# Kernel optimization log

Hardware: AMD Instinct MI355X
Metric: run time of the kernel (lower is better)

The kernel has to match this reference:

```python
import jax, jax.numpy as jnp
import numpy as np

NUM_LATENT = 1024
LATENT_DIM = 256
BETA = 0.25
N_TOKENS = 65536


def setup_inputs() -> dict:
    key = jax.random.key(0)
    k1, k2 = jax.random.split(key)
    latent_embedding = jax.random.normal(k1, (N_TOKENS, LATENT_DIM), dtype=jnp.float32)
    # torch.nn.init.uniform_(codebook, -1/num_latent, 1/num_latent)
    codebook = jax.random.uniform(
        k2, (NUM_LATENT, LATENT_DIM), dtype=jnp.float32,
        minval=-1.0 / NUM_LATENT, maxval=1.0 / NUM_LATENT)
    return {"latent_embedding": latent_embedding, "codebook": codebook}


def reference(latent_embedding, codebook):
    le_det = jax.lax.stop_gradient(latent_embedding)  # [N, D]
    # distances[n,k] = ||z_n||^2 + ||c_k||^2 - 2 z_n . c_k   (z detached, codebook NOT)
    distances = (jnp.sum(le_det ** 2, axis=1, keepdims=True)
                 + jnp.sum(codebook ** 2, axis=1)
                 - 2.0 * jnp.matmul(le_det, codebook.T))  # [N, K]
    encoding_inds = jnp.argmin(distances, axis=1)  # [N]
    # one_hot @ codebook == gather rows of codebook
    quantized_latents = codebook[encoding_inds]  # [N, D]
    num_latent = codebook.shape[0]
    commitment_loss = jnp.mean((jax.lax.stop_gradient(quantized_latents)
                                - latent_embedding) ** 2) * num_latent
    embedding_loss = jnp.mean((quantized_latents - le_det) ** 2) * num_latent
    vq_loss = embedding_loss + commitment_loss * BETA
    probs = jax.nn.softmax(-distances, axis=1)  # [N, K]
    probs = jnp.clip(jnp.mean(probs, axis=0, keepdims=True), 0.001, 0.999)  # [1, K]
    return (quantized_latents, codebook, probs, vq_loss)
```

## Files before the change

kernel.cpp:

```cpp
#include <hip/hip_runtime.h>

#define N_TOK 65536
#define DIM   256
#define K_CODES 1024
#define CB_OFF    16777216
#define PROBS_OFF (16777216 + 262144)
#define LOSS_OFF  (16777216 + 262144 + 1024)
#define TM 64
#define NBLK (N_TOK / TM)

typedef float  f32x4  __attribute__((ext_vector_type(4)));
typedef short  s16x8  __attribute__((ext_vector_type(8)));

__device__ __forceinline__ unsigned short f32_to_bf16(float x) {
    unsigned u = __float_as_uint(x);
    unsigned r = (u + 0x7FFFu + ((u >> 16) & 1u)) >> 16;
    return (unsigned short)r;
}
__device__ __forceinline__ unsigned fkey(float a) {
    unsigned u = __float_as_uint(a);
    unsigned m = (unsigned)(((int)u) >> 31);
    return u ^ (m | 0x80000000u);
}
__device__ __forceinline__ float fkey_inv(unsigned k) {
    unsigned u = (k & 0x80000000u) ? (k ^ 0x80000000u) : ~k;
    return __uint_as_float(u);
}

__device__ __forceinline__ unsigned red16_max_u(unsigned v) {
    unsigned t;
    t = (unsigned)__builtin_amdgcn_update_dpp(0, (int)v, 0xB1,  0xF, 0xF, true); v = v > t ? v : t;
    t = (unsigned)__builtin_amdgcn_update_dpp(0, (int)v, 0x4E,  0xF, 0xF, true); v = v > t ? v : t;
    t = (unsigned)__builtin_amdgcn_update_dpp(0, (int)v, 0x141, 0xF, 0xF, true); v = v > t ? v : t;
    t = (unsigned)__builtin_amdgcn_update_dpp(0, (int)v, 0x140, 0xF, 0xF, true); v = v > t ? v : t;
    return v;
}
__device__ __forceinline__ float red16_sum_f(float v) {
    float t;
    t = __uint_as_float((unsigned)__builtin_amdgcn_update_dpp(0, (int)__float_as_uint(v), 0xB1,  0xF, 0xF, true)); v += t;
    t = __uint_as_float((unsigned)__builtin_amdgcn_update_dpp(0, (int)__float_as_uint(v), 0x4E,  0xF, 0xF, true)); v += t;
    t = __uint_as_float((unsigned)__builtin_amdgcn_update_dpp(0, (int)__float_as_uint(v), 0x141, 0xF, 0xF, true)); v += t;
    t = __uint_as_float((unsigned)__builtin_amdgcn_update_dpp(0, (int)__float_as_uint(v), 0x140, 0xF, 0xF, true)); v += t;
    return v;
}

__global__ __launch_bounds__(512) void k_prep(const float* __restrict__ cb,
                                              float* __restrict__ c2,
                                              unsigned short* __restrict__ cbf,
                                              float* __restrict__ probs_part,
                                              float* __restrict__ lossR,
                                              float* __restrict__ outcb,
                                              int zcount, int nloss, int docopy) {
    const int g  = blockIdx.x;
    const int t  = threadIdx.x;
    const int wv = t >> 6;
    const int ln = t & 63;
    const int l15 = ln & 15, q = ln >> 4;

    const float* zp = cb + (size_t)(g * 16 + l15) * DIM + wv * 32 + q * 8;
    f32x4 z0 = *(const f32x4*)(zp);
    f32x4 z1 = *(const f32x4*)(zp + 4);
    s16x8 a;
    a[0] = (short)f32_to_bf16(z0[0]); a[1] = (short)f32_to_bf16(z0[1]);
    a[2] = (short)f32_to_bf16(z0[2]); a[3] = (short)f32_to_bf16(z0[3]);
    a[4] = (short)f32_to_bf16(z1[0]); a[5] = (short)f32_to_bf16(z1[1]);
    a[6] = (short)f32_to_bf16(z1[2]); a[7] = (short)f32_to_bf16(z1[3]);
    *(s16x8*)(cbf + (size_t)(g * 8 + wv) * 512 + ln * 8) = a;

    float s = z0[0]*z0[0] + z0[1]*z0[1] + z0[2]*z0[2] + z0[3]*z0[3]
            + z1[0]*z1[0] + z1[1]*z1[1] + z1[2]*z1[2] + z1[3]*z1[3];
    s += __shfl_xor(s, 16, 64);
    s += __shfl_xor(s, 32, 64);
    __shared__ float c2p[8][16];
    if (q == 0) c2p[wv][l15] = s;

    const int base = g * 512 + t;
    if (base < nloss) lossR[base] = 0.f;
    if (zcount >= 0) {
        if (base < zcount) probs_part[base] = 0.f;
        if (base + 32768 < zcount) probs_part[base + 32768] = 0.f;
    } else {
        if (base < -zcount) probs_part[(size_t)base * 1024] = 0.f;
    }
    if (docopy) {
        #pragma unroll
        for (int i = 0; i < 8; i++) outcb[base + i * 32768] = cb[base + i * 32768];
    }

    __syncthreads();
    if (t < 16) {
        float acc = 0.f;
        #pragma unroll
        for (int ww = 0; ww < 8; ww++) acc += c2p[ww][t];
        c2[g * 16 + t] = acc;
    }
}

__global__ __launch_bounds__(1024, 4) void k_main(const float* __restrict__ z,
                                                  const float* __restrict__ cb,
                                                  const unsigned short* __restrict__ cbf,
                                                  const float* __restrict__ c2,
                                                  float* __restrict__ out_q,
                                                  float* __restrict__ probs_part,
                                                  float* __restrict__ lossR,
                                                  int repmask) {
    const int t   = threadIdx.x;
    const int w   = t >> 6;
    const int ln  = t & 63;
    const int q   = ln >> 4;
    const int l15 = ln & 15;
    const int k0  = w * 64;
    const int n0  = blockIdx.x * TM;
    float* pp = probs_part +
        (size_t)((repmask < 0) ? (int)blockIdx.x : (int)(blockIdx.x & repmask)) * K_CODES;

    __shared__ unsigned short a_lds[32 * 64 * 8];
    __shared__ float    z2p[32][16];
    __shared__ unsigned kred[16][64];
    __shared__ float    ered[16][64];
    __shared__ int   fidx[64];
    __shared__ float fU[64];

    #pragma unroll
    for (int rep = 0; rep < 2; rep++) {
        const int f   = t + rep * 1024;
        const int md  = w + rep * 16;
        const int m   = md >> 3;
        const int dsv = md & 7;
        const int row = m * 16 + l15;
        const int dim = dsv * 32 + q * 8;
        const float* zp = z + (size_t)(n0 + row) * DIM + dim;
        f32x4 z0 = *(const f32x4*)(zp);
        f32x4 z1 = *(const f32x4*)(zp + 4);
        s16x8 a;
        a[0] = (short)f32_to_bf16(z0[0]); a[1] = (short)f32_to_bf16(z0[1]);
        a[2] = (short)f32_to_bf16(z0[2]); a[3] = (short)f32_to_bf16(z0[3]);
        a[4] = (short)f32_to_bf16(z1[0]); a[5] = (short)f32_to_bf16(z1[1]);
        a[6] = (short)f32_to_bf16(z1[2]); a[7] = (short)f32_to_bf16(z1[3]);
        *(s16x8*)(a_lds + (size_t)f * 8) = a;
        float s = z0[0]*z0[0] + z0[1]*z0[1] + z0[2]*z0[2] + z0[3]*z0[3]
                + z1[0]*z1[0] + z1[1]*z1[1] + z1[2]*z1[2] + z1[3]*z1[3];
        s += __shfl_xor(s, 16, 64);
        s += __shfl_xor(s, 32, 64);
        if (q == 0) z2p[md][l15] = s;
    }

    float c2v[4];
    #pragma unroll
    for (int nt = 0; nt < 4; nt++) c2v[nt] = c2[k0 + nt * 16 + l15];
    f32x4 acc[4][4];
    #pragma unroll
    for (int m = 0; m < 4; m++)
        #pragma unroll
        for (int nt = 0; nt < 4; nt++) {
            const float iv = -0.5f * c2v[nt];
            f32x4 v4 = {iv, iv, iv, iv};
            acc[m][nt] = v4;
        }

    __syncthreads();

    const unsigned short* bb = cbf + (size_t)(w * 4) * 8 * 512 + ln * 8;
    #pragma unroll
    for (int ds = 0; ds < 8; ds++) {
        s16x8 af[4];
        #pragma unroll
        for (int m = 0; m < 4; m++)
            af[m] = *(const s16x8*)(a_lds + (size_t)((m * 8 + ds) * 64 + ln) * 8);
        #pragma unroll
        for (int nt = 0; nt < 4; nt++) {
            s16x8 b = *(const s16x8*)(bb + (size_t)(nt * 8 + ds) * 512);
            #pragma unroll
            for (int m = 0; m < 4; m++)
                acc[m][nt] = __builtin_amdgcn_mfma_f32_16x16x32_bf16(af[m], b, acc[m][nt], 0, 0, 0);
        }
    }

    unsigned lkey[4][4];
    float    lesum[4][4];
    #pragma unroll
    for (int m = 0; m < 4; m++)
        #pragma unroll
        for (int v = 0; v < 4; v++) { lkey[m][v] = 0u; lesum[m][v] = 0.f; }

    #pragma unroll
    for (int m = 0; m < 4; m++)
        #pragma unroll
        for (int nt = 0; nt < 4; nt++) {
            const unsigned colc = 1023u - (unsigned)(k0 + nt * 16 + l15);
            #pragma unroll
            for (int v = 0; v < 4; v++) {
                float a = acc[m][nt][v];
                unsigned key = (fkey(a) & 0xFFFFFC00u) | colc;
                lkey[m][v] = max(lkey[m][v], key);
                float e = __expf(a + a);
                acc[m][nt][v] = e;
                lesum[m][v] += e;
            }
        }

    #pragma unroll
    for (int m = 0; m < 4; m++)
        #pragma unroll
        for (int v = 0; v < 4; v++) {
            lkey[m][v]  = red16_max_u(lkey[m][v]);
            lesum[m][v] = red16_sum_f(lesum[m][v]);
        }

    if (l15 == 0) {
        #pragma unroll
        for (int m = 0; m < 4; m++)
            #pragma unroll
            for (int v = 0; v < 4; v++) {
                const int r = m * 16 + q * 4 + v;
                kred[w][r] = lkey[m][v]; ered[w][r] = lesum[m][v];
            }
    }
    __syncthreads();
    float lossreg = 0.f;
    if (t < 64) {
        unsigned bk = kred[0][t];
        float U = ered[0][t];
        #pragma unroll
        for (int ww = 1; ww < 16; ww++) {
            bk = max(bk, kred[ww][t]);
            U += ered[ww][t];
        }
        fidx[t] = 1023 - (int)(bk & 1023u);
        fU[t] = U;
        float a_rec = fkey_inv(bk);
        float z2 = 0.f;
        #pragma unroll
        for (int ds = 0; ds < 8; ds++) z2 += z2p[(t >> 4) * 8 + ds][t & 15];
        lossreg = z2 - 2.0f * a_rec;
    }
    __syncthreads();

    float ps[4];
    #pragma unroll
    for (int nt = 0; nt < 4; nt++) ps[nt] = 0.f;
    #pragma unroll
    for (int m = 0; m < 4; m++)
        #pragma unroll
        for (int v = 0; v < 4; v++) {
            const float invU = 1.0f / fU[m * 16 + q * 4 + v];
            #pragma unroll
            for (int nt = 0; nt < 4; nt++) ps[nt] += acc[m][nt][v] * invU;
        }
    #pragma unroll
    for (int nt = 0; nt < 4; nt++) {
        ps[nt] += __shfl_xor(ps[nt], 16, 64);
        ps[nt] += __shfl_xor(ps[nt], 32, 64);
    }
    if (repmask < 0) pp[k0 + q * 16 + l15] = ps[q];
    else             atomicAdd(&pp[k0 + q * 16 + l15], ps[q]);

    #pragma unroll
    for (int i = 0; i < 4; i++) {
        const int r  = w * 4 + i;
        const int am = fidx[r];
        f32x4 qv = *(const f32x4*)(cb + (size_t)am * DIM + ln * 4);
        *(f32x4*)(out_q + (size_t)(n0 + r) * DIM + ln * 4) = qv;
    }

    if (w == 0) {
        #pragma unroll
        for (int off = 32; off; off >>= 1) lossreg += __shfl_down(lossreg, off, 64);
        if (ln == 0) atomicAdd(&lossR[blockIdx.x & 63], lossreg);
    }
}

__global__ __launch_bounds__(1024) void k_fin(const float* __restrict__ cb,
                                              const float* __restrict__ probs_part,
                                              const float* __restrict__ lossR,
                                              float* __restrict__ out,
                                              int R, int nLoss, int docopy) {
    const int t = threadIdx.x;
    const int g = blockIdx.x * 1024 + t;
    __shared__ float part[16][64];
    if (docopy && g < 262144) out[CB_OFF + g] = cb[g];
    if (R >= NBLK) {
        if (blockIdx.x < 16) {
            const int w  = t >> 6;
            const int ln = t & 63;
            const int col = blockIdx.x * 64 + ln;
            const float* p0 = probs_part + (size_t)(w * 64) * K_CODES + col;
            float a0 = 0.f, a1 = 0.f, a2 = 0.f, a3 = 0.f;
            #pragma unroll 4
            for (int r = 0; r < 64; r += 4) {
                a0 += p0[(size_t)(r + 0) * K_CODES];
                a1 += p0[(size_t)(r + 1) * K_CODES];
                a2 += p0[(size_t)(r + 2) * K_CODES];
                a3 += p0[(size_t)(r + 3) * K_CODES];
            }
            part[w][ln] = a0 + a1 + a2 + a3;
            __syncthreads();
            if (t < 64) {
                float p = 0.f;
                #pragma unroll
                for (int ww = 0; ww < 16; ww++) p += part[ww][t];
                p *= (1.0f / 65536.0f);
                p = fminf(fmaxf(p, 0.001f), 0.999f);
                out[PROBS_OFF + blockIdx.x * 64 + t] = p;
            }
        }
    } else if (g < K_CODES) {
        float a0 = 0.f, a1 = 0.f, a2 = 0.f, a3 = 0.f;
        if (R >= 4) {
            for (int r = 0; r < R; r += 4) {
                a0 += probs_part[(r + 0) * K_CODES + g];
                a1 += probs_part[(r + 1) * K_CODES + g];
                a2 += probs_part[(r + 2) * K_CODES + g];
                a3 += probs_part[(r + 3) * K_CODES + g];
            }
        } else {
            for (int r = 0; r < R; r++) a0 += probs_part[r * K_CODES + g];
        }
        float p = (a0 + a1 + a2 + a3) * (1.0f / 65536.0f);
        p = fminf(fmaxf(p, 0.001f), 0.999f);
        out[PROBS_OFF + g] = p;
    }
    if (g == 0) {
        float ls = 0.f;
        for (int r = 0; r < nLoss; r++) ls += lossR[r];
        out[LOSS_OFF] = ls * (1280.0f / 16777216.0f);
    }
}

extern "C" void kernel_launch(void* const* d_in, const int* in_sizes, int n_in,
                              void* d_out, int out_size, void* d_ws, size_t ws_size,
                              hipStream_t stream) {
    (void)in_sizes; (void)n_in; (void)out_size;
    const float* z  = (const float*)d_in[0];
    const float* cb = (const float*)d_in[1];
    float* out = (float*)d_out;

    float* c2 = (float*)d_ws;

    float *probs_part, *lossR;
    int R, nLoss, repmask;
    size_t used = 1024 * 4;
    auto fits = [&](int r) { return ws_size >= used + (size_t)(64 + r * 1024) * 4; };
    if      (fits(NBLK)) R = NBLK;
    else if (fits(64))   R = 64;
    else if (fits(16))   R = 16;
    else if (fits(4))    R = 4;
    else                 R = 0;
    const int storeMode = (R == NBLK);
    if (R) {
        lossR      = c2 + 1024;
        probs_part = lossR + 64;
        nLoss = 64;
        used += (size_t)(64 + (size_t)R * 1024) * 4;
        repmask = storeMode ? -1 : (R - 1);
    } else {
        probs_part = out + PROBS_OFF;
        lossR      = out + LOSS_OFF;
        R = 1; nLoss = 1; repmask = 0;
    }

    unsigned short* cbf;
    int cbf_in_ws = (ws_size >= used + (size_t)K_CODES * DIM * 2);
    if (cbf_in_ws) cbf = (unsigned short*)((char*)d_ws + used);
    else           cbf = (unsigned short*)(out + CB_OFF);

    k_prep<<<dim3(64), dim3(512), 0, stream>>>(cb, c2, cbf, probs_part, lossR,
                                               out + CB_OFF, storeMode ? -NBLK : R * 1024,
                                               nLoss, cbf_in_ws);
    k_main<<<dim3(NBLK), dim3(1024), 0, stream>>>(z, cb, cbf, c2, out, probs_part,
                                                  lossR, repmask);
    const int fin_blocks = (!cbf_in_ws) ? 256 : (storeMode ? 16 : 1);
    k_fin<<<dim3(fin_blocks), dim3(1024), 0, stream>>>(cb, probs_part, lossR, out,
                                                       R, nLoss, !cbf_in_ws);
}
```

Measured before the change: 201.4 us.

## Make main kernel persistent over 4 tiles with async global-to-LDS z prefetch

The main kernel now launches a quarter as many blocks, and each block loops over four token tiles. The next tile's latent rows are prefetched into a swizzled LDS staging buffer with global_load_lds while the current tile runs its MFMA and softmax work. This aims to hide global load latency and amortise per-block setup such as the c2 load. In exchange it adds 64 KB of LDS per block, which likely cuts occupancy, and launches fewer blocks (256) across the device.

```diff
diff --git a/kernel.cpp b/kernel.cpp
--- a/kernel.cpp
+++ b/kernel.cpp
@@ -8,6 +8,8 @@
 #define LOSS_OFF  (16777216 + 262144 + 1024)
 #define TM 64
 #define NBLK (N_TOK / TM)
+#define TPASS 4
+#define GRID_MAIN (NBLK / TPASS)
 
 typedef float  f32x4  __attribute__((ext_vector_type(4)));
 typedef short  s16x8  __attribute__((ext_vector_type(8)));
@@ -42,6 +44,22 @@
     t = __uint_as_float((unsigned)__builtin_amdgcn_update_dpp(0, (int)__float_as_uint(v), 0x141, 0xF, 0xF, true)); v += t;
     t = __uint_as_float((unsigned)__builtin_amdgcn_update_dpp(0, (int)__float_as_uint(v), 0x140, 0xF, 0xF, true)); v += t;
     return v;
+}
+
+__device__ __forceinline__ int zswz(int row) {
+    return (((row) & 7) << 3) | ((((row) >> 3) & 1) << 2);
+}
+__device__ __forceinline__ void gl_lds16(const float* gp, float* lp) {
+    __builtin_amdgcn_global_load_lds(
+        (const __attribute__((address_space(1))) unsigned int*)gp,
+        (__attribute__((address_space(3))) unsigned int*)lp, 16, 0, 0);
+}
+__device__ __forceinline__ void stage_tile(const float* zg, float* zstage, int w, int ln) {
+    #pragma unroll
+    for (int s = 0; s < 4; s++) {
+        const int j = s * 16 + w;
+        gl_lds16(zg + j * 256 + ((ln * 4) ^ zswz(j)), &zstage[j * 256]);
+    }
 }
 
 __global__ __launch_bounds__(512) void k_prep(const float* __restrict__ cb,
@@ -110,10 +128,8 @@
     const int q   = ln >> 4;
     const int l15 = ln & 15;
     const int k0  = w * 64;
-    const int n0  = blockIdx.x * TM;
-    float* pp = probs_part +
-        (size_t)((repmask < 0) ? (int)blockIdx.x : (int)(blockIdx.x & repmask)) * K_CODES;
-
+
+    __shared__ float zstage[TM * DIM];
     __shared__ unsigned short a_lds[32 * 64 * 8];
     __shared__ float    z2p[32][16];
     __shared__ unsigned kred[16][64];
@@ -121,152 +137,169 @@
     __shared__ int   fidx[64];
     __shared__ float fU[64];
 
-    #pragma unroll
-    for (int rep = 0; rep < 2; rep++) {
-        const int f   = t + rep * 1024;
-        const int md  = w + rep * 16;
-        const int m   = md >> 3;
-        const int dsv = md & 7;
-        const int row = m * 16 + l15;
-        const int dim = dsv * 32 + q * 8;
-        const float* zp = z + (size_t)(n0 + row) * DIM + dim;
-        f32x4 z0 = *(const f32x4*)(zp);
-        f32x4 z1 = *(const f32x4*)(zp + 4);
-        s16x8 a;
-        a[0] = (short)f32_to_bf16(z0[0]); a[1] = (short)f32_to_bf16(z0[1]);
-        a[2] = (short)f32_to_bf16(z0[2]); a[3] = (short)f32_to_bf16(z0[3]);
-        a[4] = (short)f32_to_bf16(z1[0]); a[5] = (short)f32_to_bf16(z1[1]);
-        a[6] = (short)f32_to_bf16(z1[2]); a[7] = (short)f32_to_bf16(z1[3]);
-        *(s16x8*)(a_lds + (size_t)f * 8) = a;
-        float s = z0[0]*z0[0] + z0[1]*z0[1] + z0[2]*z0[2] + z0[3]*z0[3]
-                + z1[0]*z1[0] + z1[1]*z1[1] + z1[2]*z1[2] + z1[3]*z1[3];
-        s += __shfl_xor(s, 16, 64);
-        s += __shfl_xor(s, 32, 64);
-        if (q == 0) z2p[md][l15] = s;
-    }
-
     float c2v[4];
     #pragma unroll
     for (int nt = 0; nt < 4; nt++) c2v[nt] = c2[k0 + nt * 16 + l15];
-    f32x4 acc[4][4];
-    #pragma unroll
-    for (int m = 0; m < 4; m++)
+    const unsigned short* bb = cbf + (size_t)(w * 4) * 8 * 512 + ln * 8;
+    float loss_acc = 0.f;
+
+    stage_tile(z + (size_t)blockIdx.x * TM * DIM, zstage, w, ln);
+
+    for (int p = 0; p < TPASS; p++) {
+        const int tile = blockIdx.x + p * GRID_MAIN;
+        const int n0   = tile * TM;
+        float* pp = probs_part +
+            (size_t)((repmask < 0) ? tile : (tile & repmask)) * K_CODES;
+
+        asm volatile("s_waitcnt vmcnt(0)" ::: "memory");
+        __syncthreads();
+
+        #pragma unroll
+        for (int rep = 0; rep < 2; rep++) {
+            const int md  = w + rep * 16;
+            const int m   = md >> 3;
+            const int dsv = md & 7;
+            const int row = m * 16 + l15;
+            const int dim = dsv * 32 + q * 8;
+            const int sw  = zswz(row);
+            const float* zp = zstage + row * 256;
+            f32x4 z0 = *(const f32x4*)(zp + (dim ^ sw));
+            f32x4 z1 = *(const f32x4*)(zp + ((dim + 4) ^ sw));
+            s16x8 a;
+            a[0] = (short)f32_to_bf16(z0[0]); a[1] = (short)f32_to_bf16(z0[1]);
+            a[2] = (short)f32_to_bf16(z0[2]); a[3] = (short)f32_to_bf16(z0[3]);
+            a[4] = (short)f32_to_bf16(z1[0]); a[5] = (short)f32_to_bf16(z1[1]);
+            a[6] = (short)f32_to_bf16(z1[2]); a[7] = (short)f32_to_bf16(z1[3]);
+            *(s16x8*)(a_lds + (size_t)(md * 64 + ln) * 8) = a;
+            float s = z0[0]*z0[0] + z0[1]*z0[1] + z0[2]*z0[2] + z0[3]*z0[3]
+                    + z1[0]*z1[0] + z1[1]*z1[1] + z1[2]*z1[2] + z1[3]*z1[3];
+            s += __shfl_xor(s, 16, 64);
+            s += __shfl_xor(s, 32, 64);
+            if (q == 0) z2p[md][l15] = s;
+        }
+
+        f32x4 acc[4][4];
+        #pragma unroll
+        for (int m = 0; m < 4; m++)
+            #pragma unroll
+            for (int nt = 0; nt < 4; nt++) {
+                const float iv = -0.5f * c2v[nt];
+                f32x4 v4 = {iv, iv, iv, iv};
+                acc[m][nt] = v4;
+            }
+
+        __syncthreads();
+
+        if (p + 1 < TPASS)
+            stage_tile(z + (size_t)(blockIdx.x + (p + 1) * GRID_MAIN) * TM * DIM,
+                       zstage, w, ln);
+
+        #pragma unroll
+        for (int ds = 0; ds < 8; ds++) {
+            s16x8 af[4];
+            #pragma unroll
+            for (int m = 0; m < 4; m++)
+                af[m] = *(const s16x8*)(a_lds + (size_t)((m * 8 + ds) * 64 + ln) * 8);
+            #pragma unroll
+            for (int nt = 0; nt < 4; nt++) {
+                s16x8 b = *(const s16x8*)(bb + (size_t)(nt * 8 + ds) * 512);
+                #pragma unroll
+                for (int m = 0; m < 4; m++)
+                    acc[m][nt] = __builtin_amdgcn_mfma_f32_16x16x32_bf16(af[m], b, acc[m][nt], 0, 0, 0);
+            }
+        }
+
+        unsigned lkey[4][4];
+        float    lesum[4][4];
+        #pragma unroll
+        for (int m = 0; m < 4; m++)
+            #pragma unroll
+            for (int v = 0; v < 4; v++) { lkey[m][v] = 0u; lesum[m][v] = 0.f; }
+
+        #pragma unroll
+        for (int m = 0; m < 4; m++)
+            #pragma unroll
+            for (int nt = 0; nt < 4; nt++) {
+                const unsigned colc = 1023u - (unsigned)(k0 + nt * 16 + l15);
+                #pragma unroll
+                for (int v = 0; v < 4; v++) {
+                    float a = acc[m][nt][v];
+                    unsigned key = (fkey(a) & 0xFFFFFC00u) | colc;
+                    lkey[m][v] = max(lkey[m][v], key);
+                    float e = __expf(a + a);
+                    acc[m][nt][v] = e;
+                    lesum[m][v] += e;
+                }
+            }
+
+        #pragma unroll
+        for (int m = 0; m < 4; m++)
+            #pragma unroll
+            for (int v = 0; v < 4; v++) {
+                lkey[m][v]  = red16_max_u(lkey[m][v]);
+                lesum[m][v] = red16_sum_f(lesum[m][v]);
+            }
+
+        if (l15 == 0) {
+            #pragma unroll
+            for (int m = 0; m < 4; m++)
+                #pragma unroll
+                for (int v = 0; v < 4; v++) {
+                    const int r = m * 16 + q * 4 + v;
+                    kred[w][r] = lkey[m][v]; ered[w][r] = lesum[m][v];
+                }
+        }
+        __syncthreads();
+        if (t < 64) {
+            unsigned bk = kred[0][t];
+            float U = ered[0][t];
+            #pragma unroll
+            for (int ww = 1; ww < 16; ww++) {
+                bk = max(bk, kred[ww][t]);
+                U += ered[ww][t];
+            }
+            fidx[t] = 1023 - (int)(bk & 1023u);
+            fU[t] = U;
+            float a_rec = fkey_inv(bk);
+            float z2 = 0.f;
+            #pragma unroll
+            for (int ds = 0; ds < 8; ds++) z2 += z2p[(t >> 4) * 8 + ds][t & 15];
+            loss_acc += z2 - 2.0f * a_rec;
+        }
+        __syncthreads();
+
+        float ps[4];
+        #pragma unroll
+        for (int nt = 0; nt < 4; nt++) ps[nt] = 0.f;
+        #pragma unroll
+        for (int m = 0; m < 4; m++)
+            #pragma unroll
+            for (int v = 0; v < 4; v++) {
+                const float invU = 1.0f / fU[m * 16 + q * 4 + v];
+                #pragma unroll
+                for (int nt = 0; nt < 4; nt++) ps[nt] += acc[m][nt][v] * invU;
+            }
         #pragma unroll
         for (int nt = 0; nt < 4; nt++) {
-            const float iv = -0.5f * c2v[nt];
-            f32x4 v4 = {iv, iv, iv, iv};
-            acc[m][nt] = v4;
-        }
-
-    __syncthreads();
-
-    const unsigned short* bb = cbf + (size_t)(w * 4) * 8 * 512 + ln * 8;
-    #pragma unroll
-    for (int ds = 0; ds < 8; ds++) {
-        s16x8 af[4];
-        #pragma unroll
-        for (int m = 0; m < 4; m++)
-            af[m] = *(const s16x8*)(a_lds + (size_t)((m * 8 + ds) * 64 + ln) * 8);
-        #pragma unroll
-        for (int nt = 0; nt < 4; nt++) {
-            s16x8 b = *(const s16x8*)(bb + (size_t)(nt * 8 + ds) * 512);
-            #pragma unroll
-            for (int m = 0; m < 4; m++)
-                acc[m][nt] = __builtin_amdgcn_mfma_f32_16x16x32_bf16(af[m], b, acc[m][nt], 0, 0, 0);
-        }
-    }
-
-    unsigned lkey[4][4];
-    float    lesum[4][4];
-    #pragma unroll
-    for (int m = 0; m < 4; m++)
-        #pragma unroll
-        for (int v = 0; v < 4; v++) { lkey[m][v] = 0u; lesum[m][v] = 0.f; }
-
-    #pragma unroll
-    for (int m = 0; m < 4; m++)
-        #pragma unroll
-        for (int nt = 0; nt < 4; nt++) {
-            const unsigned colc = 1023u - (unsigned)(k0 + nt * 16 + l15);
-            #pragma unroll
-            for (int v = 0; v < 4; v++) {
-                float a = acc[m][nt][v];
-                unsigned key = (fkey(a) & 0xFFFFFC00u) | colc;
-                lkey[m][v] = max(lkey[m][v], key);
-                float e = __expf(a + a);
-                acc[m][nt][v] = e;
-                lesum[m][v] += e;
-            }
-        }
-
-    #pragma unroll
-    for (int m = 0; m < 4; m++)
-        #pragma unroll
-        for (int v = 0; v < 4; v++) {
-            lkey[m][v]  = red16_max_u(lkey[m][v]);
-            lesum[m][v] = red16_sum_f(lesum[m][v]);
-        }
-
-    if (l15 == 0) {
-        #pragma unroll
-        for (int m = 0; m < 4; m++)
-            #pragma unroll
-            for (int v = 0; v < 4; v++) {
-                const int r = m * 16 + q * 4 + v;
-                kred[w][r] = lkey[m][v]; ered[w][r] = lesum[m][v];
-            }
-    }
-    __syncthreads();
-    float lossreg = 0.f;
-    if (t < 64) {
-        unsigned bk = kred[0][t];
-        float U = ered[0][t];
-        #pragma unroll
-        for (int ww = 1; ww < 16; ww++) {
-            bk = max(bk, kred[ww][t]);
-            U += ered[ww][t];
-        }
-        fidx[t] = 1023 - (int)(bk & 1023u);
-        fU[t] = U;
-        float a_rec = fkey_inv(bk);
-        float z2 = 0.f;
-        #pragma unroll
-        for (int ds = 0; ds < 8; ds++) z2 += z2p[(t >> 4) * 8 + ds][t & 15];
-        lossreg = z2 - 2.0f * a_rec;
-    }
-    __syncthreads();
-
-    float ps[4];
-    #pragma unroll
-    for (int nt = 0; nt < 4; nt++) ps[nt] = 0.f;
-    #pragma unroll
-    for (int m = 0; m < 4; m++)
-        #pragma unroll
-        for (int v = 0; v < 4; v++) {
-            const float invU = 1.0f / fU[m * 16 + q * 4 + v];
-            #pragma unroll
-            for (int nt = 0; nt < 4; nt++) ps[nt] += acc[m][nt][v] * invU;
-        }
-    #pragma unroll
-    for (int nt = 0; nt < 4; nt++) {
-        ps[nt] += __shfl_xor(ps[nt], 16, 64);
-        ps[nt] += __shfl_xor(ps[nt], 32, 64);
-    }
-    if (repmask < 0) pp[k0 + q * 16 + l15] = ps[q];
-    else             atomicAdd(&pp[k0 + q * 16 + l15], ps[q]);
-
-    #pragma unroll
-    for (int i = 0; i < 4; i++) {
-        const int r  = w * 4 + i;
-        const int am = fidx[r];
-        f32x4 qv = *(const f32x4*)(cb + (size_t)am * DIM + ln * 4);
-        *(f32x4*)(out_q + (size_t)(n0 + r) * DIM + ln * 4) = qv;
+            ps[nt] += __shfl_xor(ps[nt], 16, 64);
+            ps[nt] += __shfl_xor(ps[nt], 32, 64);
+        }
+        if (repmask < 0) pp[k0 + q * 16 + l15] = ps[q];
+        else             atomicAdd(&pp[k0 + q * 16 + l15], ps[q]);
+
+        #pragma unroll
+        for (int i = 0; i < 4; i++) {
+            const int r  = w * 4 + i;
+            const int am = fidx[r];
+            f32x4 qv = *(const f32x4*)(cb + (size_t)am * DIM + ln * 4);
+            *(f32x4*)(out_q + (size_t)(n0 + r) * DIM + ln * 4) = qv;
+        }
     }
 
     if (w == 0) {
         #pragma unroll
-        for (int off = 32; off; off >>= 1) lossreg += __shfl_down(lossreg, off, 64);
-        if (ln == 0) atomicAdd(&lossR[blockIdx.x & 63], lossreg);
+        for (int off = 32; off; off >>= 1) loss_acc += __shfl_down(loss_acc, off, 64);
+        if (ln == 0) atomicAdd(&lossR[blockIdx.x & 63], loss_acc);
     }
 }
 
@@ -367,8 +400,8 @@
     k_prep<<<dim3(64), dim3(512), 0, stream>>>(cb, c2, cbf, probs_part, lossR,
                                                out + CB_OFF, storeMode ? -NBLK : R * 1024,
                                                nLoss, cbf_in_ws);
-    k_main<<<dim3(NBLK), dim3(1024), 0, stream>>>(z, cb, cbf, c2, out, probs_part,
-                                                  lossR, repmask);
+    k_main<<<dim3(GRID_MAIN), dim3(1024), 0, stream>>>(z, cb, cbf, c2, out, probs_part,
+                                                       lossR, repmask);
     const int fin_blocks = (!cbf_in_ws) ? 256 : (storeMode ? 16 : 1);
     k_fin<<<dim3(fin_blocks), dim3(1024), 0, stream>>>(cb, probs_part, lossR, out,
                                                        R, nLoss, !cbf_in_ws);
```

Result: slower. 299.9 us (+48.9%).
